# Performance work log

Measured on AMD Instinct MI355X. Metric: run time of the kernel, lower is better.

## Reference

```python
import jax, jax.numpy as jnp
import numpy as np

# region/recall params from layer config
NUM_CLASSES = 20
NUM_ANCHORS = 5
ANCHORS = jnp.array([[1.3221, 1.73145], [3.19275, 4.00944], [5.05587, 8.09892],
                     [9.47112, 4.84053], [11.2364, 10.0071]], dtype=jnp.float32)
CONF_THRESH = 0.5
NMS_THRESH = 0.45
IOU_THRESH = 0.5
EPS = 1e-6


def setup_inputs() -> dict:
    key = jax.random.key(0)
    k1, k2 = jax.random.split(key)
    output = jax.random.normal(k1, (8, NUM_ANCHORS * (5 + NUM_CLASSES), 19, 19), dtype=jnp.float32)
    target = jax.random.uniform(k2, (8, 250), dtype=jnp.float32)  # [B, 50*5] rows: cls,cx,cy,w,h
    return {"output": output, "target": target}


def decode_region_boxes(output):
    """get_region_boxes: anchor decode. output [B, A*(5+C), H, W] -> boxes [B, A*H*W, 4] cxcywh (normalized), det_conf [B, A*H*W]."""
    B, _, H, W = output.shape
    o = output.reshape(B, NUM_ANCHORS, 5 + NUM_CLASSES, H, W)
    gx = jnp.arange(W, dtype=output.dtype)
    gy = jnp.arange(H, dtype=output.dtype)
    cx = (jax.nn.sigmoid(o[:, :, 0]) + gx[None, None, None, :]) / W
    cy = (jax.nn.sigmoid(o[:, :, 1]) + gy[None, None, :, None]) / H
    bw = jnp.exp(o[:, :, 2]) * (ANCHORS[:, 0] / W)[None, :, None, None]
    bh = jnp.exp(o[:, :, 3]) * (ANCHORS[:, 1] / H)[None, :, None, None]
    det_conf = jax.nn.sigmoid(o[:, :, 4])
    boxes = jnp.stack([cx, cy, bw, bh], axis=-1).reshape(B, -1, 4)
    return boxes, det_conf.reshape(B, -1)


def pairwise_iou(a, b):
    """bbox_iou(x1y1x2y2=False) for all pairs. a [..., Na, 4], b [..., Nb, 4] cxcywh -> [..., Na, Nb]."""
    ax1 = (a[..., 0] - a[..., 2] * 0.5)[..., :, None]
    ax2 = (a[..., 0] + a[..., 2] * 0.5)[..., :, None]
    ay1 = (a[..., 1] - a[..., 3] * 0.5)[..., :, None]
    ay2 = (a[..., 1] + a[..., 3] * 0.5)[..., :, None]
    bx1 = (b[..., 0] - b[..., 2] * 0.5)[..., None, :]
    bx2 = (b[..., 0] + b[..., 2] * 0.5)[..., None, :]
    by1 = (b[..., 1] - b[..., 3] * 0.5)[..., None, :]
    by2 = (b[..., 1] + b[..., 3] * 0.5)[..., None, :]
    uw = jnp.maximum(ax2, bx2) - jnp.minimum(ax1, bx1)
    uh = jnp.maximum(ay2, by2) - jnp.minimum(ay1, by1)
    aw = a[..., 2][..., :, None]; ah = a[..., 3][..., :, None]
    bw = b[..., 2][..., None, :]; bh = b[..., 3][..., None, :]
    cw = aw + bw - uw
    ch = ah + bh - uh
    carea = jnp.where((cw > 0) & (ch > 0), cw * ch, 0.0)
    uarea = aw * ah + bw * bh - carea
    return carea / uarea


def greedy_nms_keep(iou_mat, valid):
    """Sequential greedy NMS over conf-sorted boxes using precomputed IoU. iou_mat [N,N], valid [N] bool."""
    N = valid.shape[0]
    idx = jnp.arange(N)
    def body(i, keep):
        sup = keep[i] & (iou_mat[i] > NMS_THRESH) & (idx > i)
        return keep & (~sup)
    return jax.lax.fori_loop(0, N, body, valid)


def reference(output, target):
    B = output.shape[0]
    boxes, det = decode_region_boxes(output)              # [B,N,4], [B,N]
    # sort by det_conf descending (nms sort order)
    order = jnp.argsort(-det, axis=1)
    boxes = jnp.take_along_axis(boxes, order[..., None], axis=1)
    det = jnp.take_along_axis(det, order, axis=1)
    valid = det > CONF_THRESH                             # boxes that enter nms (conf filter in get_region_boxes)
    iou_mat = pairwise_iou(boxes, boxes)                  # [B,N,N]
    keep = jax.vmap(greedy_nms_keep)(iou_mat, valid)      # [B,N]
    proposals = jnp.sum(keep)
    # ground truth: [B,T,5] rows [cls,cx,cy,w,h]; num_gts = boxes until first cx==0
    truths = target.reshape(B, -1, 5)
    gt_valid = jnp.cumprod((truths[..., 1] != 0).astype(jnp.int32), axis=1).astype(bool)  # [B,T]
    total = jnp.sum(gt_valid)
    iou_gt = pairwise_iou(truths[..., 1:5], boxes)        # [B,T,N]
    best_iou = jnp.max(jnp.where(keep[:, None, :], iou_gt, 0.0), axis=-1)  # [B,T]
    correct = jnp.sum(gt_valid & (best_iou > IOU_THRESH))
    total_f = total.astype(jnp.float32)
    prop_f = proposals.astype(jnp.float32)
    corr_f = correct.astype(jnp.float32)
    precision = corr_f / (prop_f + EPS)
    recall = corr_f / (total_f + EPS)
    fscore = 2.0 * precision * recall / (precision + recall + EPS)
    return jnp.stack([total_f, prop_f, corr_f, precision, recall, fscore])
```

## Files before the change

### kernel.cpp

```cpp
#include <hip/hip_runtime.h>

namespace {
constexpr int NA    = 5;
constexpr int NCELL = 361;
constexpr int NBOX  = 1805;
constexpr int NBOXP = 1856;
constexpr int NT1   = 1024;
constexpr int TMAX  = 50;
constexpr float CONF_T = 0.5f;
constexpr float NMS_T  = 0.45f;
constexpr float IOU_T  = 0.5f;
constexpr int NW     = 29;
constexpr int NWMAX  = 32;
constexpr int SOA_STRIDE = NBOXP;
constexpr int SOA_ARR    = 8 * SOA_STRIDE;
constexpr int TRIW = 64 * (NW * (NW + 1) / 2);
constexpr size_t WS_COUNT = 0;
constexpr size_t WS_M     = 64;
constexpr size_t WS_SOA   = 256;
constexpr size_t WS_SUP   = 360448;
__device__ inline size_t tri_off(int w) { return (size_t)32 * w * (w + 1); }
}

__device__ __constant__ float d_anchw[NA] = {1.3221f, 3.19275f, 5.05587f, 9.47112f, 11.2364f};
__device__ __constant__ float d_anchh[NA] = {1.73145f, 4.00944f, 8.09892f, 4.84053f, 10.0071f};

__device__ inline unsigned long long rdlane64(unsigned long long v, int l) {
    unsigned lo = (unsigned)__builtin_amdgcn_readlane((int)(unsigned)(v & 0xffffffffull), l);
    unsigned hi = (unsigned)__builtin_amdgcn_readlane((int)(unsigned)(v >> 32), l);
    return ((unsigned long long)hi << 32) | lo;
}
__device__ inline void barrier_lgkm() {
    __asm__ volatile("" ::: "memory");
    __builtin_amdgcn_s_waitcnt(0xC07F);
    __builtin_amdgcn_s_barrier();
    __asm__ volatile("" ::: "memory");
}

__global__ __launch_bounds__(NT1, 1) void k_decode_sort(
    const float* __restrict__ net, float* __restrict__ soa,
    int* __restrict__ Marr, int* __restrict__ counters)
{
    __shared__ unsigned long long skey[2048];
    __shared__ float4 sbox[NBOX];
    __shared__ int sCnt;
    const int b = blockIdx.x, tid = threadIdx.x, lane = tid & 63;
    const float* op = net + (size_t)b * (NA * 25 * NCELL);
    if (tid == 0) sCnt = 0;
    if (b == 0 && tid < 4) counters[tid] = 0;
    __syncthreads();

    for (int n = tid; n < NBOX; n += NT1) {
        int a = n / NCELL;
        int r = n - a * NCELL;
        int y = r / 19;
        int x = r - y * 19;
        int base = a * 25 * NCELL + r;
        float t0 = op[base];
        float t1 = op[base + 1 * NCELL];
        float t2 = op[base + 2 * NCELL];
        float t3 = op[base + 3 * NCELL];
        float t4 = op[base + 4 * NCELL];
        float cx = (1.0f / (1.0f + expf(-t0)) + (float)x) / 19.0f;
        float cy = (1.0f / (1.0f + expf(-t1)) + (float)y) / 19.0f;
        float bw = expf(t2) * (d_anchw[a] / 19.0f);
        float bh = expf(t3) * (d_anchh[a] / 19.0f);
        float det = 1.0f / (1.0f + expf(-t4));
        sbox[n] = make_float4(cx, cy, bw, bh);
        bool valid = det > CONF_T;
        unsigned long long bm = __ballot(valid);
        int base0 = 0;
        if (lane == 0 && bm) base0 = atomicAdd(&sCnt, __popcll(bm));
        base0 = __shfl(base0, 0, 64);
        if (valid) {
            int pos = base0 + __popcll(bm & ((1ull << lane) - 1ull));
            skey[pos] = ((unsigned long long)(~__float_as_uint(det)) << 32) | (unsigned)n;
        }
    }
    __syncthreads();
    const int M = sCnt;
    int S = 64; while (S < M) S <<= 1;
    for (int n = M + tid; n < S; n += NT1) skey[n] = ~0ull;
    __syncthreads();

    unsigned long long v[8];
    const int nt8 = S >> 3;
    const int base8 = tid << 3;
    auto cas = [&](int xx, int yy, bool up) {
        unsigned long long a = v[xx], c = v[yy];
        if ((a > c) == up) { v[xx] = c; v[yy] = a; }
    };
    if (tid < nt8) {
        #pragma unroll
        for (int p = 0; p < 8; ++p) v[p] = skey[base8 + p];
        cas(0,1,true); cas(2,3,false); cas(4,5,true); cas(6,7,false);
        cas(0,2,true); cas(1,3,true); cas(4,6,false); cas(5,7,false);
        cas(0,1,true); cas(2,3,true); cas(4,5,false); cas(6,7,false);
        bool u8 = ((base8 & 8) == 0);
        cas(0,4,u8); cas(1,5,u8); cas(2,6,u8); cas(3,7,u8);
        cas(0,2,u8); cas(1,3,u8); cas(4,6,u8); cas(5,7,u8);
        cas(0,1,u8); cas(2,3,u8); cas(4,5,u8); cas(6,7,u8);
        #pragma unroll
        for (int p = 0; p < 8; ++p) skey[base8 + p] = v[p];
    }
    __syncthreads();
    for (unsigned k = 16; k <= (unsigned)S; k <<= 1) {
        for (unsigned j = k >> 1; j >= 8; j >>= 1) {
            for (unsigned m = tid; m < (unsigned)(S >> 1); m += NT1) {
                unsigned i = ((m & ~(j - 1)) << 1) | (m & (j - 1));
                unsigned p = i | j;
                bool up = ((i & k) == 0);
                unsigned long long a = skey[i], c2 = skey[p];
                if ((a > c2) == up) { skey[i] = c2; skey[p] = a; }
            }
            __syncthreads();
        }
        if (tid < nt8) {
            #pragma unroll
            for (int p = 0; p < 8; ++p) v[p] = skey[base8 + p];
            bool up = ((base8 & k) == 0);
            cas(0,4,up); cas(1,5,up); cas(2,6,up); cas(3,7,up);
            cas(0,2,up); cas(1,3,up); cas(4,6,up); cas(5,7,up);
            cas(0,1,up); cas(2,3,up); cas(4,5,up); cas(6,7,up);
            #pragma unroll
            for (int p = 0; p < 8; ++p) skey[base8 + p] = v[p];
        }
        __syncthreads();
    }

    float* X1 = soa + 0 * SOA_ARR + b * SOA_STRIDE;
    float* Y1 = soa + 1 * SOA_ARR + b * SOA_STRIDE;
    float* X2 = soa + 2 * SOA_ARR + b * SOA_STRIDE;
    float* Y2 = soa + 3 * SOA_ARR + b * SOA_STRIDE;
    float* Wd = soa + 4 * SOA_ARR + b * SOA_STRIDE;
    float* Hd = soa + 5 * SOA_ARR + b * SOA_STRIDE;
    const int mceil = (M + 63) & ~63;
    for (int p = tid; p < mceil; p += NT1) {
        float4 bx = make_float4(0.f, 0.f, 0.f, 0.f);
        if (p < M) bx = sbox[(unsigned)(skey[p] & 0xffffffffull)];
        X1[p] = bx.x - 0.5f * bx.z;
        Y1[p] = bx.y - 0.5f * bx.w;
        X2[p] = bx.x + 0.5f * bx.z;
        Y2[p] = bx.y + 0.5f * bx.w;
        Wd[p] = bx.z;
        Hd[p] = bx.w;
    }
    if (tid == 0) Marr[b] = M;
}

__global__ __launch_bounds__(256) void k_iou_maskT(
    const float* __restrict__ soa, const int* __restrict__ Marr,
    unsigned long long* __restrict__ supT)
{
    const int blk  = blockIdx.x;
    const int b    = blk & 7;
    const int g    = blk >> 3;
    const int wv   = threadIdx.x >> 6;
    const int lane = threadIdx.x & 63;
    const int M = Marr[b];
    const int i0 = g * 16 + wv * 4;
    if (i0 >= M) return;
    const float* X1 = soa + 0 * SOA_ARR + b * SOA_STRIDE;
    const float* Y1 = soa + 1 * SOA_ARR + b * SOA_STRIDE;
    const float* X2 = soa + 2 * SOA_ARR + b * SOA_STRIDE;
    const float* Y2 = soa + 3 * SOA_ARR + b * SOA_STRIDE;
    const float* Wd = soa + 4 * SOA_ARR + b * SOA_STRIDE;
    const float* Hd = soa + 5 * SOA_ARR + b * SOA_STRIDE;
    const int nch = (M + 63) >> 6;
    const int w0  = i0 >> 6;

    float ax1[4], ay1[4], ax2[4], ay2[4], aw[4], ah[4], aarea[4];
    #pragma unroll
    for (int r = 0; r < 4; ++r) {
        int ir = i0 + r; if (ir >= M) ir = M - 1;
        ax1[r] = X1[ir]; ay1[r] = Y1[ir];
        ax2[r] = X2[ir]; ay2[r] = Y2[ir];
        aw[r]  = Wd[ir]; ah[r]  = Hd[ir];
        aarea[r] = aw[r] * ah[r];
    }
    unsigned long long myw0 = 0, myw1 = 0, myw2 = 0, myw3 = 0;
    for (int w = w0; w < nch; ++w) {
        int j = (w << 6) + lane;
        float bx1 = X1[j], by1 = Y1[j];
        float bx2 = X2[j], by2 = Y2[j];
        float bw  = Wd[j], bh  = Hd[j];
        float barea = bw * bh;
        bool jok = (j < M);
        #pragma unroll
        for (int r = 0; r < 4; ++r) {
            bool pred = false;
            if (jok && j > i0 + r) {
                float uw = fmaxf(ax2[r], bx2) - fminf(ax1[r], bx1);
                float uh = fmaxf(ay2[r], by2) - fminf(ay1[r], by1);
                float cw = aw[r] + bw - uw;
                float ch = ah[r] + bh - uh;
                if (cw > 0.0f && ch > 0.0f) {
                    float ca = cw * ch;
                    float ua = aarea[r] + barea - ca;
                    pred = ca > NMS_T * ua;
                }
            }
            unsigned long long m = __ballot(pred);
            if (w == lane) {
                if      (r == 0) myw0 = m;
                else if (r == 1) myw1 = m;
                else if (r == 2) myw2 = m;
                else             myw3 = m;
            }
        }
    }
    if (lane >= w0 && lane < nch) {
        unsigned long long* dst = supT + (size_t)b * TRIW + tri_off(lane);
        dst[i0] = myw0;
        if (i0 + 1 < M) dst[i0 + 1] = myw1;
        if (i0 + 2 < M) dst[i0 + 2] = myw2;
        if (i0 + 3 < M) dst[i0 + 3] = myw3;
    }
}

__global__ __launch_bounds__(1024, 1) void k_sweep(
    const float* __restrict__ soa, const float* __restrict__ tgt,
    const int* __restrict__ Marr, const unsigned long long* __restrict__ supT,
    int* __restrict__ counters, float* __restrict__ out)
{
    __shared__ float X1s[NBOXP], Y1s[NBOXP], X2s[NBOXP], Y2s[NBOXP];
    __shared__ float Wss[NBOXP], Hss[NBOXP];
    __shared__ unsigned rmwU[2 * NWMAX];
    __shared__ unsigned long long keepw[NWMAX];
    __shared__ int sNV, sCorr, sProp;
    const int b = blockIdx.x, tid = threadIdx.x;
    const int wv = tid >> 6, lane = tid & 63;
    const int M = Marr[b];
    const int nwa = (M + 63) >> 6;
    const unsigned long long* sb = supT + (size_t)b * TRIW;

    if (tid < 2 * NWMAX) rmwU[tid] = 0u;
    if (tid < NWMAX) keepw[tid] = 0ull;
    if (tid == 0) { sCorr = 0; sProp = 0; }

    {
        int mceil = (M + 63) & ~63;
        const float* X1 = soa + 0 * SOA_ARR + b * SOA_STRIDE;
        const float* Y1 = soa + 1 * SOA_ARR + b * SOA_STRIDE;
        const float* X2 = soa + 2 * SOA_ARR + b * SOA_STRIDE;
        const float* Y2 = soa + 3 * SOA_ARR + b * SOA_STRIDE;
        const float* Wd = soa + 4 * SOA_ARR + b * SOA_STRIDE;
        const float* Hd = soa + 5 * SOA_ARR + b * SOA_STRIDE;
        for (int p = tid; p < mceil; p += 1024) {
            X1s[p] = X1[p]; Y1s[p] = Y1[p];
            X2s[p] = X2[p]; Y2s[p] = Y2[p];
            Wss[p] = Wd[p]; Hss[p] = Hd[p];
        }
    }
    if (wv == 2) {
        float cxv = (lane < TMAX) ? tgt[b * 250 + lane * 5 + 1] : 0.0f;
        unsigned long long bm = __ballot(cxv != 0.0f);
        unsigned long long inv = (~bm) & ((1ull << TMAX) - 1ull);
        if (lane == 0) sNV = inv ? (__ffsll((long long)inv) - 1) : TMAX;
    }

    const int w1 = (wv >= 1) ? wv : -1;
    const int w2 = (wv >= 1 && wv + 15 <= 28) ? (wv + 15) : -1;
    unsigned long long dAA = 0, dAB = 0, dBB = 0;
    unsigned long long curA1 = 0, curB1 = 0, curA2 = 0, curB2 = 0;
    if (wv == 0 && nwa > 0) {
        dAA = sb[tri_off(0) + lane];
        if (nwa > 1) {
            dAB = sb[tri_off(1) + lane];
            dBB = sb[tri_off(1) + 64 + lane];
        }
    }
    if (w1 >= 1 && w1 < nwa) {
        curA1 = sb[tri_off(w1) + lane];
        curB1 = sb[tri_off(w1) + 64 + lane];
    }
    if (w2 >= 1 && w2 < nwa) {
        curA2 = sb[tri_off(w2) + lane];
        curB2 = sb[tri_off(w2) + 64 + lane];
    }
    __syncthreads();

    const int nr = (nwa + 1) >> 1;
    for (int r = 0; r < nr; ++r) {
        const int tA = 2 * r, tB = 2 * r + 1;
        if (wv == 0) {
            unsigned long long curA =
                ((unsigned long long)rmwU[2 * tA + 1] << 32) | rmwU[2 * tA];
            int remA = M - (tA << 6);
            unsigned long long vmA = (remA >= 64) ? ~0ull : ((1ull << remA) - 1ull);
            unsigned long long liveA = vmA & ~curA;
            unsigned long long nxtB = 0;
            while (liveA) {
                int i = __ffsll((long long)liveA) - 1;
                unsigned long long wA = rdlane64(dAA, i);
                unsigned long long wB = rdlane64(dAB, i);
                curA |= wA;
                nxtB |= wB;
                liveA &= ~wA;
                liveA &= ~(1ull << i);
            }
            unsigned long long keepA = vmA & ~curA;
            if (lane == 0) keepw[tA] = keepA;
            if (tB < nwa) {
                unsigned long long curB =
                    (((unsigned long long)rmwU[2 * tB + 1] << 32) | rmwU[2 * tB]) | nxtB;
                int remB = M - (tB << 6);
                unsigned long long vmB = (remB >= 64) ? ~0ull : ((1ull << remB) - 1ull);
                unsigned long long liveB = vmB & ~curB;
                while (liveB) {
                    int i = __ffsll((long long)liveB) - 1;
                    unsigned long long wB = rdlane64(dBB, i);
                    curB |= wB;
                    liveB &= ~wB;
                    liveB &= ~(1ull << i);
                }
                if (lane == 0) keepw[tB] = vmB & ~curB;
            }
            int nA = tA + 2, nB = tA + 3;
            if (nA < nwa) {
                dAA = sb[tri_off(nA) + (nA << 6) + lane];
                if (nB < nwa) {
                    dAB = sb[tri_off(nB) + (nA << 6) + lane];
                    dBB = sb[tri_off(nB) + (nB << 6) + lane];
                } else { dAB = 0; dBB = 0; }
            }
        }
        barrier_lgkm();
        {
            unsigned long long kmtA = keepw[tA];
            unsigned long long kmtB = (tB < nwa) ? keepw[tB] : 0ull;
            bool keptA = (kmtA >> lane) & 1ull;
            bool keptB = (kmtB >> lane) & 1ull;
            if (w1 > tB && w1 < nwa) {
                if (keptA) {
                    unsigned lo = (unsigned)curA1, hi = (unsigned)(curA1 >> 32);
                    if (lo) atomicOr(&rmwU[2 * w1], lo);
                    if (hi) atomicOr(&rmwU[2 * w1 + 1], hi);
                }
                if (keptB) {
                    unsigned lo = (unsigned)curB1, hi = (unsigned)(curB1 >> 32);
                    if (lo) atomicOr(&rmwU[2 * w1], lo);
                    if (hi) atomicOr(&rmwU[2 * w1 + 1], hi);
                }
            }
            if (w2 > tB && w2 < nwa) {
                if (keptA) {
                    unsigned lo = (unsigned)curA2, hi = (unsigned)(curA2 >> 32);
                    if (lo) atomicOr(&rmwU[2 * w2], lo);
                    if (hi) atomicOr(&rmwU[2 * w2 + 1], hi);
                }
                if (keptB) {
                    unsigned lo = (unsigned)curB2, hi = (unsigned)(curB2 >> 32);
                    if (lo) atomicOr(&rmwU[2 * w2], lo);
                    if (hi) atomicOr(&rmwU[2 * w2 + 1], hi);
                }
            }
            int nA = tA + 2, nB = tA + 3;
            if (w1 > nB && w1 < nwa) {
                curA1 = sb[tri_off(w1) + (nA << 6) + lane];
                curB1 = sb[tri_off(w1) + (nB << 6) + lane];
            }
            if (w2 > nB && w2 < nwa) {
                curA2 = sb[tri_off(w2) + (nA << 6) + lane];
                curB2 = sb[tri_off(w2) + (nB << 6) + lane];
            }
        }
        barrier_lgkm();
    }

    if (wv == 0) {
        unsigned long long kv = (lane < NWMAX) ? keepw[lane] : 0ull;
        int pc = __popcll(kv);
        for (int d = 32; d > 0; d >>= 1) pc += __shfl_down(pc, d, 64);
        if (lane == 0) sProp = pc;
    }

    const int nv = sNV;
    for (int t = wv; t < nv; t += 16) {
        const float* g = tgt + b * 250 + t * 5;
        float gcx = g[1], gcy = g[2], gw = g[3], gh = g[4];
        float gx1 = gcx - 0.5f * gw, gx2 = gcx + 0.5f * gw;
        float gy1 = gcy - 0.5f * gh, gy2 = gcy + 0.5f * gh;
        float garea = gw * gh;
        float best = 0.0f;
        for (int j0 = 0; j0 < M; j0 += 64) {
            unsigned long long kw = keepw[j0 >> 6];
            if (kw == 0ull) continue;
            int j = j0 + lane;
            bool ok = (j < M) && ((kw >> lane) & 1ull);
            int js = (j < NBOXP) ? j : (NBOXP - 1);
            float bw = Wss[js], bh = Hss[js];
            float uw = fmaxf(gx2, X2s[js]) - fminf(gx1, X1s[js]);
            float uh = fmaxf(gy2, Y2s[js]) - fminf(gy1, Y1s[js]);
            float cww = gw + bw - uw, chh = gh + bh - uh;
            float ca = (cww > 0.0f && chh > 0.0f) ? cww * chh : 0.0f;
            float ua = garea + bw * bh - ca;
            float iou = ca / ua;
            best = fmaxf(best, ok ? iou : 0.0f);
        }
        for (int d = 32; d > 0; d >>= 1) best = fmaxf(best, __shfl_down(best, d, 64));
        if (lane == 0 && best > IOU_T) atomicAdd(&sCorr, 1);
    }
    barrier_lgkm();

    if (tid == 0) {
        atomicAdd(counters + 0, sProp);
        atomicAdd(counters + 1, sCorr);
        atomicAdd(counters + 2, sNV);
        __threadfence();
        int done = atomicAdd(counters + 3, 1);
        if (done == 7) {
            float prop  = (float)atomicAdd(counters + 0, 0);
            float corr  = (float)atomicAdd(counters + 1, 0);
            float total = (float)atomicAdd(counters + 2, 0);
            float prec = corr / (prop + 1e-6f);
            float rec  = corr / (total + 1e-6f);
            float fs   = 2.0f * prec * rec / (prec + rec + 1e-6f);
            out[0] = total;
            out[1] = prop;
            out[2] = corr;
            out[3] = prec;
            out[4] = rec;
            out[5] = fs;
        }
    }
}

extern "C" void kernel_launch(void* const* d_in, const int* in_sizes, int n_in,
                              void* d_out, int out_size, void* d_ws, size_t ws_size,
                              hipStream_t stream) {
    const float* net = (const float*)d_in[0];
    const float* tgt = (const float*)d_in[1];
    char* ws = (char*)d_ws;
    int* counters = (int*)(ws + WS_COUNT);
    int* Marr     = (int*)(ws + WS_M);
    float* soa    = (float*)(ws + WS_SOA);
    unsigned long long* supT = (unsigned long long*)(ws + WS_SUP);

    k_decode_sort<<<8, NT1, 0, stream>>>(net, soa, Marr, counters);
    int rowblocks = (NBOX + 15) / 16;
    k_iou_maskT<<<rowblocks * 8, 256, 0, stream>>>(soa, Marr, supT);
    k_sweep<<<8, 1024, 0, stream>>>(soa, tgt, Marr, supT, counters, (float*)d_out);
}
```

Before: 126.5 us.

## Fuse IoU mask and NMS sweep kernels with atomic-counter grid handoff

Merges the IoU suppression-mask kernel and the sweep kernel into one launch. The first 232 blocks of 1024 threads build the mask, with 16 waves of 4 rows each, and then increment a global counter. The last 8 blocks stage box data into shared memory, then spin on that counter before starting the sweep. This removes one kernel launch and lets the sweep blocks' setup overlap with mask construction. It relies on every mask block being scheduled before or alongside the spinning blocks, which risks deadlock or wasted spinning, and the larger mask blocks reduce occupancy compared with the earlier 256-thread blocks.

```diff
diff --git a/kernel.cpp b/kernel.cpp
--- a/kernel.cpp
+++ b/kernel.cpp
@@ -14,6 +14,8 @@
 constexpr int NWMAX  = 32;
 constexpr int SOA_STRIDE = NBOXP;
 constexpr int SOA_ARR    = 8 * SOA_STRIDE;
+constexpr int NMASKB = 29 * 8;
+constexpr int NBLK   = NMASKB + 8;
 constexpr int TRIW = 64 * (NW * (NW + 1) / 2);
 constexpr size_t WS_COUNT = 0;
 constexpr size_t WS_M     = 64;
@@ -47,7 +49,7 @@
     const int b = blockIdx.x, tid = threadIdx.x, lane = tid & 63;
     const float* op = net + (size_t)b * (NA * 25 * NCELL);
     if (tid == 0) sCnt = 0;
-    if (b == 0 && tid < 4) counters[tid] = 0;
+    if (b == 0 && tid < 8) counters[tid] = 0;
     __syncthreads();
 
     for (int n = tid; n < NBOX; n += NT1) {
@@ -148,79 +150,9 @@
     if (tid == 0) Marr[b] = M;
 }
 
-__global__ __launch_bounds__(256) void k_iou_maskT(
-    const float* __restrict__ soa, const int* __restrict__ Marr,
-    unsigned long long* __restrict__ supT)
-{
-    const int blk  = blockIdx.x;
-    const int b    = blk & 7;
-    const int g    = blk >> 3;
-    const int wv   = threadIdx.x >> 6;
-    const int lane = threadIdx.x & 63;
-    const int M = Marr[b];
-    const int i0 = g * 16 + wv * 4;
-    if (i0 >= M) return;
-    const float* X1 = soa + 0 * SOA_ARR + b * SOA_STRIDE;
-    const float* Y1 = soa + 1 * SOA_ARR + b * SOA_STRIDE;
-    const float* X2 = soa + 2 * SOA_ARR + b * SOA_STRIDE;
-    const float* Y2 = soa + 3 * SOA_ARR + b * SOA_STRIDE;
-    const float* Wd = soa + 4 * SOA_ARR + b * SOA_STRIDE;
-    const float* Hd = soa + 5 * SOA_ARR + b * SOA_STRIDE;
-    const int nch = (M + 63) >> 6;
-    const int w0  = i0 >> 6;
-
-    float ax1[4], ay1[4], ax2[4], ay2[4], aw[4], ah[4], aarea[4];
-    #pragma unroll
-    for (int r = 0; r < 4; ++r) {
-        int ir = i0 + r; if (ir >= M) ir = M - 1;
-        ax1[r] = X1[ir]; ay1[r] = Y1[ir];
-        ax2[r] = X2[ir]; ay2[r] = Y2[ir];
-        aw[r]  = Wd[ir]; ah[r]  = Hd[ir];
-        aarea[r] = aw[r] * ah[r];
-    }
-    unsigned long long myw0 = 0, myw1 = 0, myw2 = 0, myw3 = 0;
-    for (int w = w0; w < nch; ++w) {
-        int j = (w << 6) + lane;
-        float bx1 = X1[j], by1 = Y1[j];
-        float bx2 = X2[j], by2 = Y2[j];
-        float bw  = Wd[j], bh  = Hd[j];
-        float barea = bw * bh;
-        bool jok = (j < M);
-        #pragma unroll
-        for (int r = 0; r < 4; ++r) {
-            bool pred = false;
-            if (jok && j > i0 + r) {
-                float uw = fmaxf(ax2[r], bx2) - fminf(ax1[r], bx1);
-                float uh = fmaxf(ay2[r], by2) - fminf(ay1[r], by1);
-                float cw = aw[r] + bw - uw;
-                float ch = ah[r] + bh - uh;
-                if (cw > 0.0f && ch > 0.0f) {
-                    float ca = cw * ch;
-                    float ua = aarea[r] + barea - ca;
-                    pred = ca > NMS_T * ua;
-                }
-            }
-            unsigned long long m = __ballot(pred);
-            if (w == lane) {
-                if      (r == 0) myw0 = m;
-                else if (r == 1) myw1 = m;
-                else if (r == 2) myw2 = m;
-                else             myw3 = m;
-            }
-        }
-    }
-    if (lane >= w0 && lane < nch) {
-        unsigned long long* dst = supT + (size_t)b * TRIW + tri_off(lane);
-        dst[i0] = myw0;
-        if (i0 + 1 < M) dst[i0 + 1] = myw1;
-        if (i0 + 2 < M) dst[i0 + 2] = myw2;
-        if (i0 + 3 < M) dst[i0 + 3] = myw3;
-    }
-}
-
-__global__ __launch_bounds__(1024, 1) void k_sweep(
+__global__ __launch_bounds__(1024, 1) void k_mask_sweep(
     const float* __restrict__ soa, const float* __restrict__ tgt,
-    const int* __restrict__ Marr, const unsigned long long* __restrict__ supT,
+    const int* __restrict__ Marr, unsigned long long* __restrict__ supT,
     int* __restrict__ counters, float* __restrict__ out)
 {
     __shared__ float X1s[NBOXP], Y1s[NBOXP], X2s[NBOXP], Y2s[NBOXP];
@@ -228,8 +160,77 @@
     __shared__ unsigned rmwU[2 * NWMAX];
     __shared__ unsigned long long keepw[NWMAX];
     __shared__ int sNV, sCorr, sProp;
-    const int b = blockIdx.x, tid = threadIdx.x;
+    const int blk = blockIdx.x, tid = threadIdx.x;
     const int wv = tid >> 6, lane = tid & 63;
+
+    if (blk < NMASKB) {
+        const int b = blk & 7, g = blk >> 3;
+        const int M = Marr[b];
+        const int i0 = g * 64 + wv * 4;
+        if (i0 < M) {
+            const float* X1 = soa + 0 * SOA_ARR + b * SOA_STRIDE;
+            const float* Y1 = soa + 1 * SOA_ARR + b * SOA_STRIDE;
+            const float* X2 = soa + 2 * SOA_ARR + b * SOA_STRIDE;
+            const float* Y2 = soa + 3 * SOA_ARR + b * SOA_STRIDE;
+            const float* Wd = soa + 4 * SOA_ARR + b * SOA_STRIDE;
+            const float* Hd = soa + 5 * SOA_ARR + b * SOA_STRIDE;
+            const int nch = (M + 63) >> 6;
+            const int w0  = i0 >> 6;
+            float ax1[4], ay1[4], ax2[4], ay2[4], aw[4], ah[4], aarea[4];
+            #pragma unroll
+            for (int r = 0; r < 4; ++r) {
+                int ir = i0 + r; if (ir >= M) ir = M - 1;
+                ax1[r] = X1[ir]; ay1[r] = Y1[ir];
+                ax2[r] = X2[ir]; ay2[r] = Y2[ir];
+                aw[r]  = Wd[ir]; ah[r]  = Hd[ir];
+                aarea[r] = aw[r] * ah[r];
+            }
+            unsigned long long myw0 = 0, myw1 = 0, myw2 = 0, myw3 = 0;
+            for (int w = w0; w < nch; ++w) {
+                int j = (w << 6) + lane;
+                float bx1 = X1[j], by1 = Y1[j];
+                float bx2 = X2[j], by2 = Y2[j];
+                float bw  = Wd[j], bh  = Hd[j];
+                float barea = bw * bh;
+                bool jok = (j < M);
+                #pragma unroll
+                for (int r = 0; r < 4; ++r) {
+                    bool pred = false;
+                    if (jok && j > i0 + r) {
+                        float uw = fmaxf(ax2[r], bx2) - fminf(ax1[r], bx1);
+                        float uh = fmaxf(ay2[r], by2) - fminf(ay1[r], by1);
+                        float cw = aw[r] + bw - uw;
+                        float ch = ah[r] + bh - uh;
+                        if (cw > 0.0f && ch > 0.0f) {
+                            float ca = cw * ch;
+                            float ua = aarea[r] + barea - ca;
+                            pred = ca > NMS_T * ua;
+                        }
+                    }
+                    unsigned long long m = __ballot(pred);
+                    if (w == lane) {
+                        if      (r == 0) myw0 = m;
+                        else if (r == 1) myw1 = m;
+                        else if (r == 2) myw2 = m;
+                        else             myw3 = m;
+                    }
+                }
+            }
+            if (lane >= w0 && lane < nch) {
+                unsigned long long* dst = supT + (size_t)b * TRIW + tri_off(lane);
+                dst[i0] = myw0;
+                if (i0 + 1 < M) dst[i0 + 1] = myw1;
+                if (i0 + 2 < M) dst[i0 + 2] = myw2;
+                if (i0 + 3 < M) dst[i0 + 3] = myw3;
+            }
+        }
+        __threadfence();
+        __syncthreads();
+        if (tid == 0) atomicAdd(counters + 4, 1);
+        return;
+    }
+
+    const int b = blk - NMASKB;
     const int M = Marr[b];
     const int nwa = (M + 63) >> 6;
     const unsigned long long* sb = supT + (size_t)b * TRIW;
@@ -259,6 +260,12 @@
         if (lane == 0) sNV = inv ? (__ffsll((long long)inv) - 1) : TMAX;
     }
 
+    if (tid == 0) {
+        while (atomicAdd(counters + 4, 0) < NMASKB) { }
+        __threadfence();
+    }
+    __syncthreads();
+
     const int w1 = (wv >= 1) ? wv : -1;
     const int w2 = (wv >= 1 && wv + 15 <= 28) ? (wv + 15) : -1;
     unsigned long long dAA = 0, dAB = 0, dBB = 0;
@@ -278,7 +285,6 @@
         curA2 = sb[tri_off(w2) + lane];
         curB2 = sb[tri_off(w2) + 64 + lane];
     }
-    __syncthreads();
 
     const int nr = (nwa + 1) >> 1;
     for (int r = 0; r < nr; ++r) {
@@ -438,7 +444,5 @@
     unsigned long long* supT = (unsigned long long*)(ws + WS_SUP);
 
     k_decode_sort<<<8, NT1, 0, stream>>>(net, soa, Marr, counters);
-    int rowblocks = (NBOX + 15) / 16;
-    k_iou_maskT<<<rowblocks * 8, 256, 0, stream>>>(soa, Marr, supT);
-    k_sweep<<<8, 1024, 0, stream>>>(soa, tgt, Marr, supT, counters, (float*)d_out);
-}
+    k_mask_sweep<<<NBLK, 1024, 0, stream>>>(soa, tgt, Marr, supT, counters, (float*)d_out);
+}
```

Result: slower. 193.3 us (+52.8%).
